# Kernel tuning notes

Hardware: AMD Instinct MI355X
Metric: run time of the kernel (lower is better)

Reference implementation:

```python
import jax, jax.numpy as jnp
import numpy as np

B, T, CH, V, E, L = 64, 1024, 256, 32000, 64, 128  # batch, enc_len, channel, vocab, emb_dim, latent_dims


def setup_inputs() -> dict:
    key = jax.random.key(0)
    ks = jax.random.split(key, 13)
    s = 0.05  # weight init scale
    return {
        "prev_cont_vec": jax.random.normal(ks[0], (B, CH), jnp.float32),
        "F": jax.random.normal(ks[1], (B, T, CH), jnp.float32),
        "prev_char": jax.random.normal(ks[2], (B, V), jnp.float32),
        "state_h": jax.random.normal(ks[3], (B, L), jnp.float32),
        "state_c": jax.random.normal(ks[4], (B, L), jnp.float32),
        # learned parameters (all Dense layers use_bias=False)
        "Wc": jax.random.normal(ks[5], (V, E), jnp.float32) * s,
        "Wct1": jax.random.normal(ks[6], (CH, E), jnp.float32) * s,
        "Wo": jax.random.normal(ks[7], (L, V), jnp.float32) * s,
        "Wct2": jax.random.normal(ks[8], (CH, V), jnp.float32) * s,
        "lstm_kernel": jax.random.normal(ks[9], (E, 4 * L), jnp.float32) * s,
        "lstm_recurrent": jax.random.normal(ks[10], (L, 4 * L), jnp.float32) * s,
        "W_h": jax.random.normal(ks[11], (L, CH), jnp.float32) * s,
        "V_attn": jax.random.normal(ks[12], (1, 1, CH), jnp.float32) * s,
    }


def reference(prev_cont_vec, F, prev_char, state_h, state_c,
              Wc, Wct1, Wo, Wct2, lstm_kernel, lstm_recurrent, W_h, V_attn):
    # lstm input: Wc(prev_char) + Wct1(prev_cont_vec)  -> [B, E]
    lstm_inp = prev_char @ Wc + prev_cont_vec @ Wct1
    # Keras LSTMCell (no bias), gate order i, f, c, o
    z = lstm_inp @ lstm_kernel + state_h @ lstm_recurrent  # [B, 4L]
    zi, zf, zg, zo = jnp.split(z, 4, axis=-1)
    i = jax.nn.sigmoid(zi)
    f = jax.nn.sigmoid(zf)
    g = jnp.tanh(zg)
    o = jax.nn.sigmoid(zo)
    new_c = f * state_c + i * g
    new_h = o * jnp.tanh(new_c)
    # training=True branch: clip returned cell state
    new_c_out = jnp.clip(new_c, -10.0, 10.0)
    # additive attention over time axis of F [B, T, CH]
    H_tfm = (new_h @ W_h)[:, None, :]            # [B, 1, CH]
    e_t = V_attn * jnp.tanh(H_tfm + F)           # [B, T, CH]
    attn = jax.nn.softmax(e_t, axis=1)           # softmax over T, per channel
    c_t = jnp.sum(attn * F, axis=1)              # [B, CH]
    # output distribution
    O_t = jax.nn.softmax(new_h @ Wo + c_t @ Wct2, axis=1)  # [B, V]
    return (O_t, c_t, new_h, new_c_out)
```

## Files before the change

kernel.cpp:

```cpp
#include <hip/hip_runtime.h>
#include <hip/hip_bf16.h>

#define BB 64
#define TT 1024
#define CHN 256
#define VV 32000
#define EE 64
#define LL 128
#define NC1 250
#define KC1 128
#define TS 16

typedef unsigned short u16;
typedef unsigned int u32;

__device__ __forceinline__ float fast_rcp(float x) { return __builtin_amdgcn_rcpf(x); }
__device__ __forceinline__ float tanh_fast(float y) {
    float e = __expf(2.0f * y);
    return 1.0f - 2.0f * fast_rcp(1.0f + e);
}
__device__ __forceinline__ float sigmoid_fast(float x) {
    return fast_rcp(1.0f + __expf(-x));
}

__global__ __launch_bounds__(256) void k1_stage1(const float* __restrict__ A,
                                                 const float* __restrict__ Wc,
                                                 float* __restrict__ part) {
    __shared__ float sW[KC1][EE];
    __shared__ float sAT[KC1][32];
    const int kc = blockIdx.x;
    const int k0 = kc * KC1;
    const int y  = blockIdx.y;
    const int t  = threadIdx.x;

    #pragma unroll
    for (int f = t; f < 2048; f += 256)
        *(float4*)(&sW[0][0] + f * 4) = *(const float4*)(Wc + (size_t)k0 * EE + f * 4);
    {
        const int bl = t & 31;
        const int kq = t >> 5;
        const float* src = A + (size_t)(y * 32 + bl) * VV + k0 + kq * 16;
        #pragma unroll
        for (int j4 = 0; j4 < 4; ++j4) {
            float4 v = *(const float4*)(src + j4 * 4);
            sAT[kq * 16 + j4 * 4 + 0][bl] = v.x;
            sAT[kq * 16 + j4 * 4 + 1][bl] = v.y;
            sAT[kq * 16 + j4 * 4 + 2][bl] = v.z;
            sAT[kq * 16 + j4 * 4 + 3][bl] = v.w;
        }
    }
    __syncthreads();

    const int e  = t & 63;
    const int b0 = (t >> 6) * 8;
    float acc[8];
    #pragma unroll
    for (int i = 0; i < 8; ++i) acc[i] = 0.0f;

    #pragma unroll 4
    for (int k = 0; k < KC1; ++k) {
        float wt = sW[k][e];
        float4 a0 = *(const float4*)&sAT[k][b0];
        float4 a1 = *(const float4*)&sAT[k][b0 + 4];
        acc[0] = fmaf(a0.x, wt, acc[0]);
        acc[1] = fmaf(a0.y, wt, acc[1]);
        acc[2] = fmaf(a0.z, wt, acc[2]);
        acc[3] = fmaf(a0.w, wt, acc[3]);
        acc[4] = fmaf(a1.x, wt, acc[4]);
        acc[5] = fmaf(a1.y, wt, acc[5]);
        acc[6] = fmaf(a1.z, wt, acc[6]);
        acc[7] = fmaf(a1.w, wt, acc[7]);
    }
    const int gb = y * 32 + b0;
    #pragma unroll
    for (int i = 0; i < 8; ++i)
        part[((size_t)(gb + i) * NC1 + kc) * EE + e] = acc[i];
}

__global__ __launch_bounds__(512) void k2_lstm(const float* __restrict__ part,
    const float* __restrict__ pcv, const float* __restrict__ state_h,
    const float* __restrict__ state_c, const float* __restrict__ Wct1,
    const float* __restrict__ lstm_kernel, const float* __restrict__ lstm_rec,
    const float* __restrict__ W_h,
    float* __restrict__ out_newh, float* __restrict__ out_newc,
    float* __restrict__ At, float* __restrict__ Htfm) {
    __shared__ float red[8][EE];
    __shared__ float inp[EE];
    __shared__ float sh[LL];
    __shared__ float z[4 * LL];
    __shared__ float nh[LL];
    const int b = blockIdx.x;
    const int t = threadIdx.x;
    const int e  = t & 63;
    const int g  = t >> 6;

    {
        float s = 0.0f;
        for (int j = g; j < NC1; j += 8)
            s += part[((size_t)b * NC1 + j) * EE + e];
        const int c0 = g * 32;
        #pragma unroll 8
        for (int c = 0; c < 32; ++c)
            s = fmaf(pcv[b * CHN + c0 + c], Wct1[(size_t)(c0 + c) * EE + e], s);
        red[g][e] = s;
    }
    __syncthreads();
    if (t < EE) {
        float s = 0.0f;
        #pragma unroll
        for (int j = 0; j < 8; ++j) s += red[j][t];
        inp[t] = s;
    } else if (t >= 64 && t < 64 + LL) {
        sh[t - 64] = state_h[b * LL + (t - 64)];
    }
    __syncthreads();
    {
        float a = 0.0f;
        #pragma unroll 8
        for (int e2 = 0; e2 < EE; ++e2) a = fmaf(inp[e2], lstm_kernel[e2 * 512 + t], a);
        #pragma unroll 8
        for (int l = 0; l < LL; ++l) a = fmaf(sh[l], lstm_rec[l * 512 + t], a);
        z[t] = a;
    }
    __syncthreads();
    if (t < LL) {
        float zi = z[t], zf = z[LL + t], zg = z[2 * LL + t], zo = z[3 * LL + t];
        float ig = sigmoid_fast(zi);
        float fg = sigmoid_fast(zf);
        float gg = tanh_fast(zg);
        float og = sigmoid_fast(zo);
        float co = state_c[b * LL + t];
        float cn = fg * co + ig * gg;
        float hn = og * tanh_fast(cn);
        out_newc[b * LL + t] = fminf(fmaxf(cn, -10.0f), 10.0f);
        out_newh[b * LL + t] = hn;
        At[t * BB + b] = hn;
        nh[t] = hn;
    }
    __syncthreads();
    if (t < CHN) {
        float a = 0.0f;
        #pragma unroll 8
        for (int l = 0; l < LL; ++l) a = fmaf(nh[l], W_h[l * CHN + t], a);
        Htfm[b * CHN + t] = a;
    }
}

__global__ __launch_bounds__(256) void k3_attn(const float* __restrict__ F,
    const float* __restrict__ Htfm, const float* __restrict__ Vattn,
    float* __restrict__ pS, float* __restrict__ pW) {
    __shared__ float4 sS[256];
    __shared__ float4 sW[256];
    const int b    = blockIdx.x;
    const int ts   = blockIdx.y;
    const int lane = threadIdx.x & 63;
    const int w    = threadIdx.x >> 6;
    const int ch   = lane * 4;

    float4 h = *(const float4*)(Htfm + b * CHN + ch);
    float4 v = *(const float4*)(Vattn + ch);
    float s0 = 0, s1 = 0, s2 = 0, s3 = 0;
    float a0 = 0, a1 = 0, a2 = 0, a3 = 0;

    const float* Fp = F + ((size_t)b * TT + ts * (TT / TS) + w * 16) * CHN + ch;
    float4 cur = *(const float4*)(Fp);
    #pragma unroll
    for (int t = 0; t < 16; ++t) {
        float4 nxt;
        if (t < 15) nxt = *(const float4*)(Fp + (size_t)(t + 1) * CHN);
        float e0 = __expf(v.x * tanh_fast(h.x + cur.x));
        float e1 = __expf(v.y * tanh_fast(h.y + cur.y));
        float e2 = __expf(v.z * tanh_fast(h.z + cur.z));
        float e3 = __expf(v.w * tanh_fast(h.w + cur.w));
        s0 += e0; s1 += e1; s2 += e2; s3 += e3;
        a0 = fmaf(e0, cur.x, a0); a1 = fmaf(e1, cur.y, a1);
        a2 = fmaf(e2, cur.z, a2); a3 = fmaf(e3, cur.w, a3);
        cur = nxt;
    }
    sS[threadIdx.x] = make_float4(s0, s1, s2, s3);
    sW[threadIdx.x] = make_float4(a0, a1, a2, a3);
    __syncthreads();
    if (threadIdx.x < 64) {
        float4 S = sS[threadIdx.x];
        float4 W = sW[threadIdx.x];
        #pragma unroll
        for (int j = 1; j < 4; ++j) {
            float4 s = sS[j * 64 + threadIdx.x];
            float4 q = sW[j * 64 + threadIdx.x];
            S.x += s.x; S.y += s.y; S.z += s.z; S.w += s.w;
            W.x += q.x; W.y += q.y; W.z += q.z; W.w += q.w;
        }
        int base = (b * TS + ts) * CHN + threadIdx.x * 4;
        *(float4*)(pS + base) = S;
        *(float4*)(pW + base) = W;
    }
}

__global__ __launch_bounds__(256) void k4_combine(const float* __restrict__ pS,
    const float* __restrict__ pW, float* __restrict__ out_ct, float* __restrict__ At) {
    const int b = blockIdx.x;
    const int ch = threadIdx.x;
    float S = 0.0f, W = 0.0f;
    #pragma unroll
    for (int j = 0; j < TS; ++j) {
        int idx = (b * TS + j) * CHN + ch;
        S += pS[idx];
        W += pW[idx];
    }
    float c = W / S;
    out_ct[b * CHN + ch] = c;
    At[(LL + ch) * BB + b] = c;
}

#define K5_FMA(XW) \
    { float4 x = *(const float4*)a; float4 zz = *(const float4*)(a + 4); \
      acc[0].x = fmaf(x.x, XW.x, acc[0].x); acc[0].y = fmaf(x.x, XW.y, acc[0].y); \
      acc[1].x = fmaf(x.y, XW.x, acc[1].x); acc[1].y = fmaf(x.y, XW.y, acc[1].y); \
      acc[2].x = fmaf(x.z, XW.x, acc[2].x); acc[2].y = fmaf(x.z, XW.y, acc[2].y); \
      acc[3].x = fmaf(x.w, XW.x, acc[3].x); acc[3].y = fmaf(x.w, XW.y, acc[3].y); \
      acc[4].x = fmaf(zz.x, XW.x, acc[4].x); acc[4].y = fmaf(zz.x, XW.y, acc[4].y); \
      acc[5].x = fmaf(zz.y, XW.x, acc[5].x); acc[5].y = fmaf(zz.y, XW.y, acc[5].y); \
      acc[6].x = fmaf(zz.z, XW.x, acc[6].x); acc[6].y = fmaf(zz.z, XW.y, acc[6].y); \
      acc[7].x = fmaf(zz.w, XW.x, acc[7].x); acc[7].y = fmaf(zz.w, XW.y, acc[7].y); }

__device__ __forceinline__ void k5_phase(const float* __restrict__ W, int kn,
    const float* sAt, float2 acc[8]) {
    float2 wa[8], wb[8];
    #pragma unroll
    for (int j = 0; j < 8; ++j) wa[j] = *(const float2*)(W + (size_t)j * VV);
    for (int k = 0; k < kn; k += 16) {
        #pragma unroll
        for (int j = 0; j < 8; ++j) wb[j] = *(const float2*)(W + (size_t)(k + 8 + j) * VV);
        #pragma unroll
        for (int j = 0; j < 8; ++j) {
            const float* a = sAt + (size_t)(k + j) * 32;
            K5_FMA(wa[j]);
        }
        if (k + 16 < kn) {
            #pragma unroll
            for (int j = 0; j < 8; ++j) wa[j] = *(const float2*)(W + (size_t)(k + 16 + j) * VV);
        }
        #pragma unroll
        for (int j = 0; j < 8; ++j) {
            const float* a = sAt + (size_t)(k + 8 + j) * 32;
            K5_FMA(wb[j]);
        }
    }
}

__global__ __launch_bounds__(256) void k5_logits(const float* __restrict__ Wo,
    const float* __restrict__ Wct2, const float* __restrict__ At,
    float* __restrict__ outO, float* __restrict__ psum) {
    __shared__ float sAt[384][32];
    const int y = blockIdx.y;
    const int t = threadIdx.x;

    #pragma unroll
    for (int f = t; f < 3072; f += 256) {
        int k  = f >> 3;
        int c4 = (f & 7) * 4;
        *(float4*)&sAt[k][c4] = *(const float4*)(At + (size_t)k * BB + y * 32 + c4);
    }
    __syncthreads();

    const int lane = t & 63;
    const int v2   = blockIdx.x * 128 + lane * 2;
    const int w8   = (t >> 6) * 8;
    float2 acc[8];
    #pragma unroll
    for (int i = 0; i < 8; ++i) acc[i] = make_float2(0.0f, 0.0f);

    k5_phase(Wo + v2, LL, &sAt[0][0] + w8, acc);
    k5_phase(Wct2 + v2, CHN, &sAt[LL][0] + w8, acc);

    const int gb = y * 32 + w8;
    float ps[8];
    #pragma unroll
    for (int i = 0; i < 8; ++i) {
        float2 ex = make_float2(__expf(acc[i].x), __expf(acc[i].y));
        *(float2*)(outO + (size_t)(gb + i) * VV + v2) = ex;
        float s = ex.x + ex.y;
        #pragma unroll
        for (int m = 32; m > 0; m >>= 1) s += __shfl_xor(s, m, 64);
        ps[i] = s;
    }
    if (lane == 0) {
        #pragma unroll
        for (int i = 0; i < 8; ++i) psum[blockIdx.x * BB + gb + i] = ps[i];
    }
}

__global__ __launch_bounds__(256) void k5b_rowsum(const float* __restrict__ psum,
                                                  float* __restrict__ rowsum) {
    __shared__ float red[256];
    const int t = threadIdx.x;
    const int b = t & 63;
    const int q = t >> 6;
    float s = 0.0f;
    for (int x = q; x < NC1; x += 4) s += psum[x * BB + b];
    red[t] = s;
    __syncthreads();
    if (t < 64) rowsum[b] = red[b] + red[64 + b] + red[128 + b] + red[192 + b];
}

__global__ __launch_bounds__(256) void k5c_norm(float* __restrict__ O,
                                                const float* __restrict__ rowsum) {
    const int gid = blockIdx.x * 256 + threadIdx.x;
    float4* O4 = (float4*)O;
    const u32 row = ((u32)gid * 4u) / (u32)VV;
    const float inv = fast_rcp(rowsum[row]);
    float4 f = O4[gid];
    f.x *= inv; f.y *= inv; f.z *= inv; f.w *= inv;
    O4[gid] = f;
}

extern "C" void kernel_launch(void* const* d_in, const int* in_sizes, int n_in,
                              void* d_out, int out_size, void* d_ws, size_t ws_size,
                              hipStream_t stream) {
    (void)in_sizes; (void)n_in; (void)out_size; (void)ws_size;
    const float* pcv       = (const float*)d_in[0];
    const float* F         = (const float*)d_in[1];
    const float* prev_char = (const float*)d_in[2];
    const float* state_h   = (const float*)d_in[3];
    const float* state_c   = (const float*)d_in[4];
    const float* Wc        = (const float*)d_in[5];
    const float* Wct1      = (const float*)d_in[6];
    const float* Wo        = (const float*)d_in[7];
    const float* Wct2      = (const float*)d_in[8];
    const float* lstm_k    = (const float*)d_in[9];
    const float* lstm_r    = (const float*)d_in[10];
    const float* W_h       = (const float*)d_in[11];
    const float* Vattn     = (const float*)d_in[12];

    float* outO  = (float*)d_out;
    float* outCt = outO + (size_t)BB * VV;
    float* outH  = outCt + (size_t)BB * CHN;
    float* outC  = outH + (size_t)BB * LL;

    float* ws     = (float*)d_ws;
    float* part   = ws;
    float* pS     = part + (size_t)NC1 * BB * EE;
    float* pW     = pS + (size_t)BB * TS * CHN;
    float* At     = pW + (size_t)BB * TS * CHN;
    float* Htfm   = At + (LL + CHN) * BB;
    float* psum   = Htfm + (size_t)BB * CHN;
    float* rowsum = psum + (size_t)NC1 * BB;

    hipLaunchKernelGGL(k1_stage1, dim3(NC1, 2), dim3(256), 0, stream, prev_char, Wc, part);
    hipLaunchKernelGGL(k2_lstm, dim3(BB), dim3(512), 0, stream, part, pcv, state_h,
                       state_c, Wct1, lstm_k, lstm_r, W_h, outH, outC, At, Htfm);
    hipLaunchKernelGGL(k3_attn, dim3(BB, TS), dim3(256), 0, stream, F, Htfm, Vattn, pS, pW);
    hipLaunchKernelGGL(k4_combine, dim3(BB), dim3(256), 0, stream, pS, pW, outCt, At);
    hipLaunchKernelGGL(k5_logits, dim3(NC1, 2), dim3(256), 0, stream, Wo, Wct2, At, outO, psum);
    hipLaunchKernelGGL(k5b_rowsum, dim3(1), dim3(256), 0, stream, psum, rowsum);
    hipLaunchKernelGGL(k5c_norm, dim3((BB * VV / 4) / 256), dim3(256), 0, stream, outO, rowsum);
}
```

Measured before the change: 252.6 us.

## Compute logits GEMM with bf16 MFMA and pre-packed bf16 activations

Replaces the FP32 FMA logits kernel with a bf16 32x32x16 MFMA path. The new_h and c_t activations are packed as bf16 pairs in a k-major buffer by the LSTM and combine kernels, and weights are truncated to bf16 in registers. This removes the shared-memory staging and the scalar FMA work, leaving the kernel bound by weight bandwidth. In exchange it loses precision (bf16 inputs with truncated weights) ahead of an exp-based softmax, and the per-lane weight loads are now 4-byte strided rather than float2.

```diff
diff --git a/kernel.cpp b/kernel.cpp
--- a/kernel.cpp
+++ b/kernel.cpp
@@ -13,6 +13,8 @@
 
 typedef unsigned short u16;
 typedef unsigned int u32;
+typedef __attribute__((ext_vector_type(8))) short short8;
+typedef __attribute__((ext_vector_type(16))) float f32x16;
 
 __device__ __forceinline__ float fast_rcp(float x) { return __builtin_amdgcn_rcpf(x); }
 __device__ __forceinline__ float tanh_fast(float y) {
@@ -21,6 +23,13 @@
 }
 __device__ __forceinline__ float sigmoid_fast(float x) {
     return fast_rcp(1.0f + __expf(-x));
+}
+__device__ __forceinline__ u16 f2bf(float f) {
+    u32 u = __float_as_uint(f);
+    return (u16)((u + 0x7fffu + ((u >> 16) & 1u)) >> 16);
+}
+__device__ __forceinline__ u32 pack_bf2(float lo, float hi) {
+    return (u32)f2bf(lo) | ((u32)f2bf(hi) << 16);
 }
 
 __global__ __launch_bounds__(256) void k1_stage1(const float* __restrict__ A,
@@ -83,7 +92,7 @@
     const float* __restrict__ lstm_kernel, const float* __restrict__ lstm_rec,
     const float* __restrict__ W_h,
     float* __restrict__ out_newh, float* __restrict__ out_newc,
-    float* __restrict__ At, float* __restrict__ Htfm) {
+    u32* __restrict__ Apk, float* __restrict__ Htfm) {
     __shared__ float red[8][EE];
     __shared__ float inp[EE];
     __shared__ float sh[LL];
@@ -134,7 +143,6 @@
         float hn = og * tanh_fast(cn);
         out_newc[b * LL + t] = fminf(fmaxf(cn, -10.0f), 10.0f);
         out_newh[b * LL + t] = hn;
-        At[t * BB + b] = hn;
         nh[t] = hn;
     }
     __syncthreads();
@@ -143,6 +151,9 @@
         #pragma unroll 8
         for (int l = 0; l < LL; ++l) a = fmaf(nh[l], W_h[l * CHN + t], a);
         Htfm[b * CHN + t] = a;
+    } else if (t >= CHN && t < CHN + 64) {
+        const int k2i = t - CHN;
+        Apk[(size_t)k2i * BB + b] = pack_bf2(nh[2 * k2i], nh[2 * k2i + 1]);
     }
 }
 
@@ -197,7 +208,8 @@
 }
 
 __global__ __launch_bounds__(256) void k4_combine(const float* __restrict__ pS,
-    const float* __restrict__ pW, float* __restrict__ out_ct, float* __restrict__ At) {
+    const float* __restrict__ pW, float* __restrict__ out_ct, u32* __restrict__ Apk) {
+    __shared__ float sc[CHN];
     const int b = blockIdx.x;
     const int ch = threadIdx.x;
     float S = 0.0f, W = 0.0f;
@@ -209,85 +221,91 @@
     }
     float c = W / S;
     out_ct[b * CHN + ch] = c;
-    At[(LL + ch) * BB + b] = c;
-}
-
-#define K5_FMA(XW) \
-    { float4 x = *(const float4*)a; float4 zz = *(const float4*)(a + 4); \
-      acc[0].x = fmaf(x.x, XW.x, acc[0].x); acc[0].y = fmaf(x.x, XW.y, acc[0].y); \
-      acc[1].x = fmaf(x.y, XW.x, acc[1].x); acc[1].y = fmaf(x.y, XW.y, acc[1].y); \
-      acc[2].x = fmaf(x.z, XW.x, acc[2].x); acc[2].y = fmaf(x.z, XW.y, acc[2].y); \
-      acc[3].x = fmaf(x.w, XW.x, acc[3].x); acc[3].y = fmaf(x.w, XW.y, acc[3].y); \
-      acc[4].x = fmaf(zz.x, XW.x, acc[4].x); acc[4].y = fmaf(zz.x, XW.y, acc[4].y); \
-      acc[5].x = fmaf(zz.y, XW.x, acc[5].x); acc[5].y = fmaf(zz.y, XW.y, acc[5].y); \
-      acc[6].x = fmaf(zz.z, XW.x, acc[6].x); acc[6].y = fmaf(zz.z, XW.y, acc[6].y); \
-      acc[7].x = fmaf(zz.w, XW.x, acc[7].x); acc[7].y = fmaf(zz.w, XW.y, acc[7].y); }
-
-__device__ __forceinline__ void k5_phase(const float* __restrict__ W, int kn,
-    const float* sAt, float2 acc[8]) {
-    float2 wa[8], wb[8];
-    #pragma unroll
-    for (int j = 0; j < 8; ++j) wa[j] = *(const float2*)(W + (size_t)j * VV);
-    for (int k = 0; k < kn; k += 16) {
-        #pragma unroll
-        for (int j = 0; j < 8; ++j) wb[j] = *(const float2*)(W + (size_t)(k + 8 + j) * VV);
-        #pragma unroll
-        for (int j = 0; j < 8; ++j) {
-            const float* a = sAt + (size_t)(k + j) * 32;
-            K5_FMA(wa[j]);
+    sc[ch] = c;
+    __syncthreads();
+    if (ch < 128)
+        Apk[(size_t)(64 + ch) * BB + b] = pack_bf2(sc[2 * ch], sc[2 * ch + 1]);
+}
+
+__global__ __launch_bounds__(256) void k5_logits(const float* __restrict__ Wo,
+    const float* __restrict__ Wct2, const u32* __restrict__ Apk,
+    float* __restrict__ outO, float* __restrict__ psum) {
+    __shared__ float rp[4][32];
+    const int t    = threadIdx.x;
+    const int lane = t & 63;
+    const int wv   = t >> 6;
+    const int m    = lane & 31;
+    const int kq   = lane >> 5;
+    const int y    = blockIdx.y;
+    const int n0   = blockIdx.x * 128 + wv * 32;
+    const int gb0  = y * 32;
+
+    u32 af[24][4];
+    #pragma unroll
+    for (int tt = 0; tt < 24; ++tt) {
+        #pragma unroll
+        for (int r = 0; r < 4; ++r)
+            af[tt][r] = Apk[(size_t)(tt * 8 + kq * 4 + r) * BB + gb0 + m];
+    }
+
+    f32x16 acc = {0.0f, 0.0f, 0.0f, 0.0f, 0.0f, 0.0f, 0.0f, 0.0f,
+                  0.0f, 0.0f, 0.0f, 0.0f, 0.0f, 0.0f, 0.0f, 0.0f};
+
+    float wbuf[2][8];
+    {
+        const float* c0 = Wo + (size_t)(kq * 8) * VV + n0 + m;
+        #pragma unroll
+        for (int j = 0; j < 8; ++j) wbuf[0][j] = c0[(size_t)j * VV];
+    }
+
+    #pragma unroll
+    for (int tt = 0; tt < 24; ++tt) {
+        if (tt < 23) {
+            const int kn = (tt + 1) * 16 + kq * 8;
+            const float* cn = (kn < LL ? Wo + (size_t)kn * VV
+                                       : Wct2 + (size_t)(kn - LL) * VV) + n0 + m;
+            #pragma unroll
+            for (int j = 0; j < 8; ++j) wbuf[(tt + 1) & 1][j] = cn[(size_t)j * VV];
         }
-        if (k + 16 < kn) {
-            #pragma unroll
-            for (int j = 0; j < 8; ++j) wa[j] = *(const float2*)(W + (size_t)(k + 16 + j) * VV);
+        short8 a, b;
+        #pragma unroll
+        for (int r = 0; r < 4; ++r) {
+            u32 lo = __float_as_uint(wbuf[tt & 1][2 * r]);
+            u32 hi = __float_as_uint(wbuf[tt & 1][2 * r + 1]);
+            u32 bp = (lo >> 16) | (hi & 0xffff0000u);
+            u32 ap = af[tt][r];
+            a[2 * r]     = (short)(ap & 0xffff);
+            a[2 * r + 1] = (short)(ap >> 16);
+            b[2 * r]     = (short)(bp & 0xffff);
+            b[2 * r + 1] = (short)(bp >> 16);
         }
-        #pragma unroll
-        for (int j = 0; j < 8; ++j) {
-            const float* a = sAt + (size_t)(k + 8 + j) * 32;
-            K5_FMA(wb[j]);
-        }
-    }
-}
-
-__global__ __launch_bounds__(256) void k5_logits(const float* __restrict__ Wo,
-    const float* __restrict__ Wct2, const float* __restrict__ At,
-    float* __restrict__ outO, float* __restrict__ psum) {
-    __shared__ float sAt[384][32];
-    const int y = blockIdx.y;
-    const int t = threadIdx.x;
-
-    #pragma unroll
-    for (int f = t; f < 3072; f += 256) {
-        int k  = f >> 3;
-        int c4 = (f & 7) * 4;
-        *(float4*)&sAt[k][c4] = *(const float4*)(At + (size_t)k * BB + y * 32 + c4);
-    }
-    __syncthreads();
-
-    const int lane = t & 63;
-    const int v2   = blockIdx.x * 128 + lane * 2;
-    const int w8   = (t >> 6) * 8;
-    float2 acc[8];
-    #pragma unroll
-    for (int i = 0; i < 8; ++i) acc[i] = make_float2(0.0f, 0.0f);
-
-    k5_phase(Wo + v2, LL, &sAt[0][0] + w8, acc);
-    k5_phase(Wct2 + v2, CHN, &sAt[LL][0] + w8, acc);
-
-    const int gb = y * 32 + w8;
-    float ps[8];
-    #pragma unroll
-    for (int i = 0; i < 8; ++i) {
-        float2 ex = make_float2(__expf(acc[i].x), __expf(acc[i].y));
-        *(float2*)(outO + (size_t)(gb + i) * VV + v2) = ex;
-        float s = ex.x + ex.y;
-        #pragma unroll
-        for (int m = 32; m > 0; m >>= 1) s += __shfl_xor(s, m, 64);
-        ps[i] = s;
-    }
-    if (lane == 0) {
-        #pragma unroll
-        for (int i = 0; i < 8; ++i) psum[blockIdx.x * BB + gb + i] = ps[i];
-    }
+        acc = __builtin_amdgcn_mfma_f32_32x32x16_bf16(a, b, acc, 0, 0, 0);
+    }
+
+    float ex[16];
+    #pragma unroll
+    for (int r = 0; r < 16; ++r) {
+        const int row = (r & 3) + 8 * (r >> 2) + 4 * kq;
+        ex[r] = __expf(acc[r]);
+        outO[(size_t)(gb0 + row) * VV + n0 + m] = ex[r];
+    }
+    #pragma unroll
+    for (int r = 0; r < 16; ++r) {
+        float s = ex[r];
+        s += __shfl_xor(s, 1, 64);  s += __shfl_xor(s, 2, 64);
+        s += __shfl_xor(s, 4, 64);  s += __shfl_xor(s, 8, 64);
+        s += __shfl_xor(s, 16, 64);
+        ex[r] = s;
+    }
+    if (m == 0) {
+        #pragma unroll
+        for (int r = 0; r < 16; ++r)
+            rp[wv][(r & 3) + 8 * (r >> 2) + 4 * kq] = ex[r];
+    }
+    __syncthreads();
+    if (t < 32)
+        psum[(size_t)blockIdx.x * BB + gb0 + t] =
+            rp[0][t] + rp[1][t] + rp[2][t] + rp[3][t];
 }
 
 __global__ __launch_bounds__(256) void k5b_rowsum(const float* __restrict__ psum,
@@ -341,17 +359,17 @@
     float* part   = ws;
     float* pS     = part + (size_t)NC1 * BB * EE;
     float* pW     = pS + (size_t)BB * TS * CHN;
-    float* At     = pW + (size_t)BB * TS * CHN;
-    float* Htfm   = At + (LL + CHN) * BB;
+    float* Htfm   = pW + (size_t)BB * TS * CHN;
     float* psum   = Htfm + (size_t)BB * CHN;
     float* rowsum = psum + (size_t)NC1 * BB;
+    u32*   Apk    = (u32*)(rowsum + BB);
 
     hipLaunchKernelGGL(k1_stage1, dim3(NC1, 2), dim3(256), 0, stream, prev_char, Wc, part);
     hipLaunchKernelGGL(k2_lstm, dim3(BB), dim3(512), 0, stream, part, pcv, state_h,
-                       state_c, Wct1, lstm_k, lstm_r, W_h, outH, outC, At, Htfm);
+                       state_c, Wct1, lstm_k, lstm_r, W_h, outH, outC, Apk, Htfm);
     hipLaunchKernelGGL(k3_attn, dim3(BB, TS), dim3(256), 0, stream, F, Htfm, Vattn, pS, pW);
-    hipLaunchKernelGGL(k4_combine, dim3(BB), dim3(256), 0, stream, pS, pW, outCt, At);
-    hipLaunchKernelGGL(k5_logits, dim3(NC1, 2), dim3(256), 0, stream, Wo, Wct2, At, outO, psum);
+    hipLaunchKernelGGL(k4_combine, dim3(BB), dim3(256), 0, stream, pS, pW, outCt, Apk);
+    hipLaunchKernelGGL(k5_logits, dim3(NC1, 2), dim3(256), 0, stream, Wo, Wct2, Apk, outO, psum);
     hipLaunchKernelGGL(k5b_rowsum, dim3(1), dim3(256), 0, stream, psum, rowsum);
     hipLaunchKernelGGL(k5c_norm, dim3((BB * VV / 4) / 256), dim3(256), 0, stream, outO, rowsum);
 }
```

After: 233.7 us. 1.08x faster.
